# Performance work log

Measured on AMD Instinct MI355X. Metric: run time of the kernel, lower is better.

The kernel has to match this reference:

```python
import jax, jax.numpy as jnp
import numpy as np

B, D_BYTES, R, S, NSEG, OUT_DIM = 8, 128, 4096, 32768, 1024, 512
D_BITS = 8 * D_BYTES  # 1024


def setup_inputs() -> dict:
    key = jax.random.key(0)
    ks = jax.random.split(key, 9)
    u8 = lambda k, shape: jax.random.randint(k, shape, 0, 256, dtype=jnp.int32).astype(jnp.uint8)
    Q = u8(ks[0], (B, D_BYTES))
    Q_ok = u8(ks[1], (B, D_BYTES))
    refs = u8(ks[2], (R, D_BYTES))
    ok_pos = u8(ks[3], (R, D_BYTES))
    ref2seg = jax.random.randint(ks[4], (S,), 0, R, dtype=jnp.int32)
    segments = jnp.sort(jax.random.randint(ks[5], (S,), 0, NSEG, dtype=jnp.int32))
    W_o = jax.random.normal(ks[6], (D_BITS, OUT_DIM), dtype=jnp.float32) * (1.0 / np.sqrt(D_BITS))
    b_o = jnp.zeros((OUT_DIM,), dtype=jnp.float32)
    return {"Q": Q, "Q_ok": Q_ok, "refs": refs, "ok_pos": ok_pos,
            "ref2seg": ref2seg, "segments": segments, "N": NSEG,
            "W_o": W_o, "b_o": b_o}


def reference(Q, Q_ok, refs, ok_pos, ref2seg, segments, N, W_o, b_o):
    # values: unpack packed reference bit-sequences once: (R, d_bits) uint8
    values = jnp.unpackbits(refs, axis=1)

    def per_query(q, q_ok):
        # popcount sequence similarity, normalized by non-gap overlap length
        ok = jnp.sum(jax.lax.population_count(jnp.bitwise_and(q_ok, ok_pos)), axis=1)      # (R,)
        match = jnp.sum(jax.lax.population_count(jnp.bitwise_and(q, refs)), axis=1)        # (R,)
        dists = match / ok                                                                  # (R,) float32
        # numerically-stable segment softmax over ragged neighborhoods
        applied = jnp.take(dists, ref2seg)                                                  # (S,)
        mx = jnp.take(jax.ops.segment_max(applied, segments, num_segments=N), segments)
        e = applied - mx
        norm = jnp.take(jnp.log(jax.ops.segment_sum(jnp.exp(e), segments, num_segments=N)), segments)
        scores = jnp.exp(e - norm)                                                          # (S,)
        # gather values along edges, weight, scatter-sum into segments
        av = jnp.take(values, ref2seg, axis=0) * scores[:, None]                            # (S, d_bits)
        return jax.ops.segment_sum(av, segments, num_segments=N)                            # (N, d_bits)

    V = jax.vmap(per_query)(Q, Q_ok)        # (B, N, d_bits)
    return V @ W_o + b_o                     # (B, N, out_dim)
```

## Files before the change

kernel.cpp:

```cpp
#include <hip/hip_runtime.h>

#define B_Q   8
#define DB    128
#define R_REF 4096
#define S_EDGE 32768
#define NSEG  1024
#define DBITS 1024
#define OUTD  512

#define NB_WCONV 128
#define NB_DIST 8192
#define NB_BOUNDS 4
#define TILE_E 256

typedef __bf16 bf16_t;
typedef bf16_t bf16x8 __attribute__((ext_vector_type(8)));
typedef float  f32x4  __attribute__((ext_vector_type(4)));
typedef unsigned int u32;

__device__ inline unsigned short f2bf(float f){
  unsigned int u = __builtin_bit_cast(unsigned int, f);
  u = (u + 0x7fffu + ((u >> 16) & 1u)) >> 16;
  return (unsigned short)u;
}

__device__ __forceinline__ void gl_lds16(const unsigned short* g, unsigned short* l){
  __builtin_amdgcn_global_load_lds((const __attribute__((address_space(1))) u32*)g,
                                   (__attribute__((address_space(3))) u32*)l, 16, 0, 0);
}

__global__ __launch_bounds__(256) void k_prep(const float* __restrict__ W,
                                              unsigned short* __restrict__ WT,
                                              const int* __restrict__ refs,
                                              const int* __restrict__ Q,
                                              const int* __restrict__ Qok,
                                              const int* __restrict__ okpos,
                                              float* __restrict__ distsT,
                                              const int* __restrict__ segments,
                                              int* __restrict__ segstart){
  __shared__ float tile[64][65];
  const int bid = blockIdx.x;
  const int tid = threadIdx.x;

  if (bid < NB_WCONV){
    const int k0 = (bid & 15) * 64, o0 = (bid >> 4) * 64;
    const int tr = tid >> 6, tc = tid & 63;
    #pragma unroll
    for (int i = 0; i < 16; ++i)
      tile[tr + i*4][tc] = W[(size_t)(k0 + tr + i*4) * OUTD + o0 + tc];
    __syncthreads();
    #pragma unroll
    for (int i = 0; i < 16; ++i)
      WT[(size_t)(o0 + tr + i*4) * DBITS + k0 + tc] = f2bf(tile[tc][tr + i*4]);
  } else if (bid < NB_WCONV + NB_DIST){
    int pair = (bid - NB_WCONV) * 4 + (tid >> 6);
    int l = tid & 63;
    int b = pair >> 12;
    int r = pair & 4095;
    int q0 = Q[b*DB + l],    q1 = Q[b*DB + 64 + l];
    int a0 = Qok[b*DB + l],  a1 = Qok[b*DB + 64 + l];
    int f0 = refs[r*DB + l], f1 = refs[r*DB + 64 + l];
    int p0 = okpos[r*DB + l],p1 = okpos[r*DB + 64 + l];
    int m = __popc(q0 & f0) + __popc(q1 & f1);
    int o = __popc(a0 & p0) + __popc(a1 & p1);
    int v = m | (o << 16);
    #pragma unroll
    for (int off = 32; off; off >>= 1) v += __shfl_down(v, off);
    if (l == 0) distsT[r * 8 + b] = (float)(v & 0xffff) / (float)(v >> 16);
  } else {
    int n = (bid - NB_WCONV - NB_DIST) * 256 + tid;
    int lo = 0, hi = S_EDGE;
    #pragma unroll 1
    while (lo < hi){ int mid = (lo + hi) >> 1; if (segments[mid] < n) lo = mid + 1; else hi = mid; }
    segstart[n] = lo;
    if (n == 0) segstart[NSEG] = S_EDGE;
  }
}

__global__ __launch_bounds__(256) void k_ugemm(const int* __restrict__ refs,
                                               const unsigned short* __restrict__ WT,
                                               unsigned short* __restrict__ U){
  __shared__ unsigned short AS[2 * 64 * 128];
  __shared__ unsigned short BS[2 * 64 * 128];
  const int tid = threadIdx.x;
  const int w = tid >> 6, l = tid & 63;
  const int tm = blockIdx.x * 64, tn = blockIdx.y * 64;
  const int wm = (w & 1) * 32, wn = (w >> 1) * 32;
  const int lr = l & 15, kq = l >> 4;

  f32x4 acc[2][2] = {};
  int cur = 0;

  #define STAGE_B(buf, K0)                                                                 \
    do {                                                                                   \
      _Pragma("unroll")                                                                    \
      for (int c = 0; c < 4; ++c){                                                         \
        int idx = c * 256 + tid;                                                           \
        int row = idx >> 4, ch = idx & 15;                                                 \
        int gch = ch ^ (row & 15);                                                         \
        gl_lds16(WT + (size_t)(tn + row) * DBITS + (K0) + gch*8,                           \
                 BS + (buf)*8192 + row*128 + ch*8);                                        \
      }                                                                                    \
    } while (0)

  #define STAGE_A(buf, K0)                                                                 \
    do {                                                                                   \
      int row = tid >> 2, j0 = (tid & 3) * 4;                                              \
      int4 rv = *(const int4*)(refs + (size_t)(tm + row) * DB + (K0)/8 + j0);              \
      const int rx = row & 15;                                                             \
      int vv[4] = {rv.x, rv.y, rv.z, rv.w};                                                \
      _Pragma("unroll")                                                                    \
      for (int j = 0; j < 4; ++j){                                                         \
        u32 v = (u32)vv[j];                                                                \
        uint4 o;                                                                           \
        u32* wp = (u32*)&o;                                                                \
        _Pragma("unroll")                                                                  \
        for (int i2 = 0; i2 < 4; ++i2){                                                    \
          u32 b0 = (v >> (7 - 2*i2)) & 1u;                                                 \
          u32 b1 = (v >> (6 - 2*i2)) & 1u;                                                 \
          wp[i2] = b0 * 0x3F80u | ((b1 * 0x3F80u) << 16);                                  \
        }                                                                                  \
        int lch = (j0 + j) ^ rx;                                                           \
        *(uint4*)(AS + (buf)*8192 + row*128 + lch*8) = o;                                  \
      }                                                                                    \
    } while (0)

  STAGE_B(0, 0);
  STAGE_A(0, 0);
  __syncthreads();

  for (int s = 0; s < 8; ++s){
    if (s < 7){ STAGE_B(cur ^ 1, (s + 1) * 128); STAGE_A(cur ^ 1, (s + 1) * 128); }
    #pragma unroll
    for (int kk = 0; kk < 4; ++kk){
      bf16x8 af[2], bfr[2];
      #pragma unroll
      for (int m = 0; m < 2; ++m){
        int row = wm + m*16 + lr;
        int ch  = (kk*4 + kq) ^ (row & 15);
        af[m] = __builtin_bit_cast(bf16x8, *(const uint4*)(AS + cur*8192 + row*128 + ch*8));
      }
      #pragma unroll
      for (int n = 0; n < 2; ++n){
        int row = wn + n*16 + lr;
        int ch  = (kk*4 + kq) ^ (row & 15);
        bfr[n] = __builtin_bit_cast(bf16x8, *(const uint4*)(BS + cur*8192 + row*128 + ch*8));
      }
      #pragma unroll
      for (int m = 0; m < 2; ++m)
        #pragma unroll
        for (int n = 0; n < 2; ++n)
          acc[m][n] = __builtin_amdgcn_mfma_f32_16x16x32_bf16(af[m], bfr[n], acc[m][n], 0, 0, 0);
    }
    __syncthreads();
    cur ^= 1;
  }
  #undef STAGE_A
  #undef STAGE_B

  #pragma unroll
  for (int n = 0; n < 2; ++n)
    #pragma unroll
    for (int m = 0; m < 2; ++m){
      int row = tm + wm + m*16 + kq*4;
      int col = tn + wn + n*16 + lr;
      #pragma unroll
      for (int q = 0; q < 4; ++q)
        U[(size_t)(row + q) * OUTD + col] = f2bf(acc[m][n][q]);
    }
}

__global__ __launch_bounds__(256) void k_scat(const float* __restrict__ distsT,
                                              const int* __restrict__ ref2seg,
                                              const int* __restrict__ segstart,
                                              const unsigned short* __restrict__ U,
                                              const float* __restrict__ bo,
                                              float* __restrict__ out){
  __shared__ float mbs[8], ibs[8];
  __shared__ float scl[TILE_E * 8];
  __shared__ int   rix[TILE_E];
  const int n = blockIdx.x;
  const int t = threadIdx.x;

  const int start = segstart[n], end = segstart[n + 1];

  const float b0c = bo[2*t], b1c = bo[2*t + 1];
  float* op = out + (size_t)n * OUTD + 2*t;

  if (start >= end){
    #pragma unroll
    for (int j = 0; j < 8; ++j){
      op[(size_t)j * NSEG * OUTD]     = b0c;
      op[(size_t)j * NSEG * OUTD + 1] = b1c;
    }
    return;
  }

  if (t < 64){
    const int sb = t >> 3, es = t & 7;
    float m = -1e30f, s = 0.f;
    for (int e = start + es; e < end; e += 8){
      float d = distsT[ref2seg[e] * 8 + sb];
      float mn = fmaxf(m, d);
      s = s * __expf(m - mn) + __expf(d - mn);
      m = mn;
    }
    #pragma unroll
    for (int msk = 1; msk < 8; msk <<= 1){
      float mo = __shfl_xor(m, msk), so = __shfl_xor(s, msk);
      float mn = fmaxf(m, mo);
      s = s * __expf(m - mn) + so * __expf(mo - mn);
      m = mn;
    }
    if (es == 0){ mbs[sb] = m; ibs[sb] = 1.0f / s; }
  }
  __syncthreads();

  float acc[8][2];
  #pragma unroll
  for (int j = 0; j < 8; ++j){ acc[j][0] = 0.f; acc[j][1] = 0.f; }

  for (int e0 = start; e0 < end; e0 += TILE_E){
    const int cnt = min(TILE_E, end - e0);
    for (int i = t; i < cnt * 8; i += 256){
      int e = e0 + (i >> 3), b = i & 7;
      int r = ref2seg[e];
      if (b == 0) rix[i >> 3] = r;
      scl[i] = __expf(distsT[r*8 + b] - mbs[b]) * ibs[b];
    }
    __syncthreads();

    #pragma unroll 4
    for (int e = 0; e < cnt; ++e){
      int r = rix[e];
      float4 s0 = *(const float4*)(scl + e*8);
      float4 s1 = *(const float4*)(scl + e*8 + 4);
      u32 uu = *(const u32*)(U + ((size_t)r << 9) + 2*t);
      float ux = __builtin_bit_cast(float, uu << 16);
      float uy = __builtin_bit_cast(float, uu & 0xffff0000u);
      float ss[8] = {s0.x, s0.y, s0.z, s0.w, s1.x, s1.y, s1.z, s1.w};
      #pragma unroll
      for (int j = 0; j < 8; ++j){
        acc[j][0] += ss[j] * ux;
        acc[j][1] += ss[j] * uy;
      }
    }
    __syncthreads();
  }

  #pragma unroll
  for (int j = 0; j < 8; ++j){
    op[(size_t)j * NSEG * OUTD]     = acc[j][0] + b0c;
    op[(size_t)j * NSEG * OUTD + 1] = acc[j][1] + b1c;
  }
}

extern "C" void kernel_launch(void* const* d_in, const int* in_sizes, int n_in,
                              void* d_out, int out_size, void* d_ws, size_t ws_size,
                              hipStream_t stream) {
  const int*   Q        = (const int*)d_in[0];
  const int*   Qok      = (const int*)d_in[1];
  const int*   refs     = (const int*)d_in[2];
  const int*   okpos    = (const int*)d_in[3];
  const int*   ref2seg  = (const int*)d_in[4];
  const int*   segments = (const int*)d_in[5];
  const float* W        = (const float*)d_in[7];
  const float* bo       = (const float*)d_in[8];
  float* out = (float*)d_out;

  char* ws = (char*)d_ws;
  unsigned short* WT       = (unsigned short*)ws;
  float*          distsT   = (float*)(ws + (1u<<20));
  int*            segstart = (int*)(ws + (1u<<20) + (160u<<10));
  unsigned short* U        = (unsigned short*)(ws + (11u<<20));

  k_prep <<<NB_WCONV + NB_DIST + NB_BOUNDS, 256, 0, stream>>>(W, WT, refs, Q, Qok, okpos,
                                                              distsT, segments, segstart);
  k_ugemm<<<dim3(R_REF/64, OUTD/64), 256, 0, stream>>>(refs, WT, U);
  k_scat <<<NSEG, 256, 0, stream>>>(distsT, ref2seg, segstart, U, bo, out);
}
```

Before: 43.43 us.

## Fuse W conversion and U GEMM into the prep kernel, dropping WT staging

The separate W transpose/bf16 conversion and the U GEMM kernel are merged into one front kernel. GEMM blocks now read fp32 W directly, convert to bf16 and write it transposed and swizzled into LDS, so the WT workspace round trip and one kernel launch go away. The distance blocks now handle four refs per wave to cut block count. In exchange, every GEMM block repeats the W conversion, B staging uses plain loads and scattered 4-byte LDS writes instead of direct global-to-LDS copies, and GEMM blocks share the launch with distance and bounds blocks.

```diff
diff --git a/kernel.cpp b/kernel.cpp
--- a/kernel.cpp
+++ b/kernel.cpp
@@ -8,8 +8,8 @@
 #define DBITS 1024
 #define OUTD  512
 
-#define NB_WCONV 128
-#define NB_DIST 8192
+#define NB_GEMM 512
+#define NB_DIST 2048
 #define NB_BOUNDS 4
 #define TILE_E 256
 
@@ -24,150 +24,143 @@
   return (unsigned short)u;
 }
 
-__device__ __forceinline__ void gl_lds16(const unsigned short* g, unsigned short* l){
-  __builtin_amdgcn_global_load_lds((const __attribute__((address_space(1))) u32*)g,
-                                   (__attribute__((address_space(3))) u32*)l, 16, 0, 0);
-}
-
-__global__ __launch_bounds__(256) void k_prep(const float* __restrict__ W,
-                                              unsigned short* __restrict__ WT,
-                                              const int* __restrict__ refs,
-                                              const int* __restrict__ Q,
-                                              const int* __restrict__ Qok,
-                                              const int* __restrict__ okpos,
-                                              float* __restrict__ distsT,
-                                              const int* __restrict__ segments,
-                                              int* __restrict__ segstart){
-  __shared__ float tile[64][65];
+__global__ __launch_bounds__(256) void k_front(const float* __restrict__ W,
+                                               const int* __restrict__ refs,
+                                               const int* __restrict__ Q,
+                                               const int* __restrict__ Qok,
+                                               const int* __restrict__ okpos,
+                                               float* __restrict__ distsT,
+                                               const int* __restrict__ segments,
+                                               int* __restrict__ segstart,
+                                               unsigned short* __restrict__ U){
+  __shared__ unsigned short AS[2 * 8192];
+  __shared__ unsigned short BS[2 * 8192];
   const int bid = blockIdx.x;
   const int tid = threadIdx.x;
 
-  if (bid < NB_WCONV){
-    const int k0 = (bid & 15) * 64, o0 = (bid >> 4) * 64;
-    const int tr = tid >> 6, tc = tid & 63;
-    #pragma unroll
-    for (int i = 0; i < 16; ++i)
-      tile[tr + i*4][tc] = W[(size_t)(k0 + tr + i*4) * OUTD + o0 + tc];
+  if (bid < NB_GEMM){
+    const int tn = (bid & 7) * 64, tm = (bid >> 3) * 64;
+    const int w = tid >> 6, l = tid & 63;
+    const int wm = (w & 1) * 32, wn = (w >> 1) * 32;
+    const int lr = l & 15, kq = l >> 4;
+
+    f32x4 acc[2][2] = {};
+    int cur = 0;
+
+    #define STAGE_A(buf, K0)                                                               \
+      do {                                                                                 \
+        int row = tid >> 2, j0 = (tid & 3) * 4;                                            \
+        int4 rv = *(const int4*)(refs + (size_t)(tm + row) * DB + (K0)/8 + j0);            \
+        const int rx = row & 15;                                                           \
+        int vv[4] = {rv.x, rv.y, rv.z, rv.w};                                              \
+        _Pragma("unroll")                                                                  \
+        for (int j = 0; j < 4; ++j){                                                       \
+          u32 v = (u32)vv[j];                                                              \
+          uint4 o;                                                                         \
+          u32* wp = (u32*)&o;                                                              \
+          _Pragma("unroll")                                                                \
+          for (int i2 = 0; i2 < 4; ++i2){                                                  \
+            u32 b0 = (v >> (7 - 2*i2)) & 1u;                                               \
+            u32 b1 = (v >> (6 - 2*i2)) & 1u;                                               \
+            wp[i2] = b0 * 0x3F80u | ((b1 * 0x3F80u) << 16);                                \
+          }                                                                                \
+          int lch = (j0 + j) ^ rx;                                                         \
+          *(uint4*)(AS + (buf)*8192 + row*128 + lch*8) = o;                                \
+        }                                                                                  \
+      } while (0)
+
+    #define STAGE_BW(buf, K0)                                                              \
+      do {                                                                                 \
+        _Pragma("unroll")                                                                  \
+        for (int c = 0; c < 4; ++c){                                                       \
+          int idx = c * 256 + tid;                                                         \
+          int kpair = idx >> 4, oq = idx & 15;                                             \
+          int k = (K0) + kpair * 2;                                                        \
+          float4 w0 = *(const float4*)(W + (size_t)k * OUTD + tn + oq * 4);                \
+          float4 w1 = *(const float4*)(W + (size_t)(k + 1) * OUTD + tn + oq * 4);          \
+          int krel = kpair * 2;                                                            \
+          int gch = krel >> 3, kb = krel & 7;                                              \
+          float wa0[4] = {w0.x, w0.y, w0.z, w0.w};                                         \
+          float wa1[4] = {w1.x, w1.y, w1.z, w1.w};                                         \
+          _Pragma("unroll")                                                                \
+          for (int j = 0; j < 4; ++j){                                                     \
+            int row = oq * 4 + j;                                                          \
+            int ch = gch ^ (row & 15);                                                     \
+            u32 val = (u32)f2bf(wa0[j]) | ((u32)f2bf(wa1[j]) << 16);                       \
+            *(u32*)(BS + (buf)*8192 + row*128 + ch*8 + kb) = val;                          \
+          }                                                                                \
+        }                                                                                  \
+      } while (0)
+
+    STAGE_BW(0, 0);
+    STAGE_A(0, 0);
     __syncthreads();
-    #pragma unroll
-    for (int i = 0; i < 16; ++i)
-      WT[(size_t)(o0 + tr + i*4) * DBITS + k0 + tc] = f2bf(tile[tc][tr + i*4]);
-  } else if (bid < NB_WCONV + NB_DIST){
-    int pair = (bid - NB_WCONV) * 4 + (tid >> 6);
-    int l = tid & 63;
-    int b = pair >> 12;
-    int r = pair & 4095;
-    int q0 = Q[b*DB + l],    q1 = Q[b*DB + 64 + l];
-    int a0 = Qok[b*DB + l],  a1 = Qok[b*DB + 64 + l];
-    int f0 = refs[r*DB + l], f1 = refs[r*DB + 64 + l];
-    int p0 = okpos[r*DB + l],p1 = okpos[r*DB + 64 + l];
-    int m = __popc(q0 & f0) + __popc(q1 & f1);
-    int o = __popc(a0 & p0) + __popc(a1 & p1);
-    int v = m | (o << 16);
-    #pragma unroll
-    for (int off = 32; off; off >>= 1) v += __shfl_down(v, off);
-    if (l == 0) distsT[r * 8 + b] = (float)(v & 0xffff) / (float)(v >> 16);
+
+    for (int s = 0; s < 8; ++s){
+      if (s < 7){ STAGE_BW(cur ^ 1, (s + 1) * 128); STAGE_A(cur ^ 1, (s + 1) * 128); }
+      #pragma unroll
+      for (int kk = 0; kk < 4; ++kk){
+        bf16x8 af[2], bfr[2];
+        #pragma unroll
+        for (int m = 0; m < 2; ++m){
+          int row = wm + m*16 + lr;
+          int ch  = (kk*4 + kq) ^ (row & 15);
+          af[m] = __builtin_bit_cast(bf16x8, *(const uint4*)(AS + cur*8192 + row*128 + ch*8));
+        }
+        #pragma unroll
+        for (int n = 0; n < 2; ++n){
+          int row = wn + n*16 + lr;
+          int ch  = (kk*4 + kq) ^ (row & 15);
+          bfr[n] = __builtin_bit_cast(bf16x8, *(const uint4*)(BS + cur*8192 + row*128 + ch*8));
+        }
+        #pragma unroll
+        for (int m = 0; m < 2; ++m)
+          #pragma unroll
+          for (int n = 0; n < 2; ++n)
+            acc[m][n] = __builtin_amdgcn_mfma_f32_16x16x32_bf16(af[m], bfr[n], acc[m][n], 0, 0, 0);
+      }
+      __syncthreads();
+      cur ^= 1;
+    }
+    #undef STAGE_A
+    #undef STAGE_BW
+
+    #pragma unroll
+    for (int n = 0; n < 2; ++n)
+      #pragma unroll
+      for (int m = 0; m < 2; ++m){
+        int row = tm + wm + m*16 + kq*4;
+        int col = tn + wn + n*16 + lr;
+        #pragma unroll
+        for (int q = 0; q < 4; ++q)
+          U[(size_t)(row + q) * OUTD + col] = f2bf(acc[m][n][q]);
+      }
+  } else if (bid < NB_GEMM + NB_DIST){
+    const int w = tid >> 6, l = tid & 63;
+    const int base = (bid - NB_GEMM) * 16 + w * 4;
+    const int b = base >> 12;
+    const int q0 = Q[b*DB + l],   q1 = Q[b*DB + 64 + l];
+    const int a0 = Qok[b*DB + l], a1 = Qok[b*DB + 64 + l];
+    #pragma unroll
+    for (int i = 0; i < 4; ++i){
+      int r = (base + i) & 4095;
+      int f0 = refs[r*DB + l], f1 = refs[r*DB + 64 + l];
+      int p0 = okpos[r*DB + l],p1 = okpos[r*DB + 64 + l];
+      int m = __popc(q0 & f0) + __popc(q1 & f1);
+      int o = __popc(a0 & p0) + __popc(a1 & p1);
+      int v = m | (o << 16);
+      #pragma unroll
+      for (int off = 32; off; off >>= 1) v += __shfl_down(v, off);
+      if (l == 0) distsT[r * 8 + b] = (float)(v & 0xffff) / (float)(v >> 16);
+    }
   } else {
-    int n = (bid - NB_WCONV - NB_DIST) * 256 + tid;
+    int n = (bid - NB_GEMM - NB_DIST) * 256 + tid;
     int lo = 0, hi = S_EDGE;
     #pragma unroll 1
     while (lo < hi){ int mid = (lo + hi) >> 1; if (segments[mid] < n) lo = mid + 1; else hi = mid; }
     segstart[n] = lo;
     if (n == 0) segstart[NSEG] = S_EDGE;
   }
-}
-
-__global__ __launch_bounds__(256) void k_ugemm(const int* __restrict__ refs,
-                                               const unsigned short* __restrict__ WT,
-                                               unsigned short* __restrict__ U){
-  __shared__ unsigned short AS[2 * 64 * 128];
-  __shared__ unsigned short BS[2 * 64 * 128];
-  const int tid = threadIdx.x;
-  const int w = tid >> 6, l = tid & 63;
-  const int tm = blockIdx.x * 64, tn = blockIdx.y * 64;
-  const int wm = (w & 1) * 32, wn = (w >> 1) * 32;
-  const int lr = l & 15, kq = l >> 4;
-
-  f32x4 acc[2][2] = {};
-  int cur = 0;
-
-  #define STAGE_B(buf, K0)                                                                 \
-    do {                                                                                   \
-      _Pragma("unroll")                                                                    \
-      for (int c = 0; c < 4; ++c){                                                         \
-        int idx = c * 256 + tid;                                                           \
-        int row = idx >> 4, ch = idx & 15;                                                 \
-        int gch = ch ^ (row & 15);                                                         \
-        gl_lds16(WT + (size_t)(tn + row) * DBITS + (K0) + gch*8,                           \
-                 BS + (buf)*8192 + row*128 + ch*8);                                        \
-      }                                                                                    \
-    } while (0)
-
-  #define STAGE_A(buf, K0)                                                                 \
-    do {                                                                                   \
-      int row = tid >> 2, j0 = (tid & 3) * 4;                                              \
-      int4 rv = *(const int4*)(refs + (size_t)(tm + row) * DB + (K0)/8 + j0);              \
-      const int rx = row & 15;                                                             \
-      int vv[4] = {rv.x, rv.y, rv.z, rv.w};                                                \
-      _Pragma("unroll")                                                                    \
-      for (int j = 0; j < 4; ++j){                                                         \
-        u32 v = (u32)vv[j];                                                                \
-        uint4 o;                                                                           \
-        u32* wp = (u32*)&o;                                                                \
-        _Pragma("unroll")                                                                  \
-        for (int i2 = 0; i2 < 4; ++i2){                                                    \
-          u32 b0 = (v >> (7 - 2*i2)) & 1u;                                                 \
-          u32 b1 = (v >> (6 - 2*i2)) & 1u;                                                 \
-          wp[i2] = b0 * 0x3F80u | ((b1 * 0x3F80u) << 16);                                  \
-        }                                                                                  \
-        int lch = (j0 + j) ^ rx;                                                           \
-        *(uint4*)(AS + (buf)*8192 + row*128 + lch*8) = o;                                  \
-      }                                                                                    \
-    } while (0)
-
-  STAGE_B(0, 0);
-  STAGE_A(0, 0);
-  __syncthreads();
-
-  for (int s = 0; s < 8; ++s){
-    if (s < 7){ STAGE_B(cur ^ 1, (s + 1) * 128); STAGE_A(cur ^ 1, (s + 1) * 128); }
-    #pragma unroll
-    for (int kk = 0; kk < 4; ++kk){
-      bf16x8 af[2], bfr[2];
-      #pragma unroll
-      for (int m = 0; m < 2; ++m){
-        int row = wm + m*16 + lr;
-        int ch  = (kk*4 + kq) ^ (row & 15);
-        af[m] = __builtin_bit_cast(bf16x8, *(const uint4*)(AS + cur*8192 + row*128 + ch*8));
-      }
-      #pragma unroll
-      for (int n = 0; n < 2; ++n){
-        int row = wn + n*16 + lr;
-        int ch  = (kk*4 + kq) ^ (row & 15);
-        bfr[n] = __builtin_bit_cast(bf16x8, *(const uint4*)(BS + cur*8192 + row*128 + ch*8));
-      }
-      #pragma unroll
-      for (int m = 0; m < 2; ++m)
-        #pragma unroll
-        for (int n = 0; n < 2; ++n)
-          acc[m][n] = __builtin_amdgcn_mfma_f32_16x16x32_bf16(af[m], bfr[n], acc[m][n], 0, 0, 0);
-    }
-    __syncthreads();
-    cur ^= 1;
-  }
-  #undef STAGE_A
-  #undef STAGE_B
-
-  #pragma unroll
-  for (int n = 0; n < 2; ++n)
-    #pragma unroll
-    for (int m = 0; m < 2; ++m){
-      int row = tm + wm + m*16 + kq*4;
-      int col = tn + wn + n*16 + lr;
-      #pragma unroll
-      for (int q = 0; q < 4; ++q)
-        U[(size_t)(row + q) * OUTD + col] = f2bf(acc[m][n][q]);
-    }
 }
 
 __global__ __launch_bounds__(256) void k_scat(const float* __restrict__ distsT,
@@ -269,13 +262,11 @@
   float* out = (float*)d_out;
 
   char* ws = (char*)d_ws;
-  unsigned short* WT       = (unsigned short*)ws;
   float*          distsT   = (float*)(ws + (1u<<20));
   int*            segstart = (int*)(ws + (1u<<20) + (160u<<10));
   unsigned short* U        = (unsigned short*)(ws + (11u<<20));
 
-  k_prep <<<NB_WCONV + NB_DIST + NB_BOUNDS, 256, 0, stream>>>(W, WT, refs, Q, Qok, okpos,
-                                                              distsT, segments, segstart);
-  k_ugemm<<<dim3(R_REF/64, OUTD/64), 256, 0, stream>>>(refs, WT, U);
+  k_front<<<NB_GEMM + NB_DIST + NB_BOUNDS, 256, 0, stream>>>(W, refs, Q, Qok, okpos,
+                                                             distsT, segments, segstart, U);
   k_scat <<<NSEG, 256, 0, stream>>>(distsT, ref2seg, segstart, U, bo, out);
 }
```

New measurement: 48.78 us. 12.3% more time.
